# Kernel tuning notes

Measured on AMD Instinct MI355X. Metric: run time of the kernel, lower is better.

The kernel has to match this reference:

```python
import jax, jax.numpy as jnp
import numpy as np
import math

B, S, DIM = 2, 2048, 2048
H, KV, HD = 16, 1, 128  # query heads, kv heads, head dim


def setup_inputs() -> dict:
    key = jax.random.key(0)
    ks = jax.random.split(key, 6)
    std = 0.02
    return {
        "hidden_states": jax.random.normal(ks[0], (B, S, DIM), jnp.float32),
        "attention_mask": jnp.zeros((B, 1, S, S), jnp.float32),
        "wq": jax.random.normal(ks[1], (DIM, H * HD), jnp.float32) * std,
        "bq": jnp.zeros((H * HD,), jnp.float32),
        "wk": jax.random.normal(ks[2], (DIM, KV * HD), jnp.float32) * std,
        "bk": jnp.zeros((KV * HD,), jnp.float32),
        "wv": jax.random.normal(ks[3], (DIM, KV * HD), jnp.float32) * std,
        "bv": jnp.zeros((KV * HD,), jnp.float32),
        "wo": jax.random.normal(ks[4], (H * HD, DIM), jnp.float32) * std,
        "bo": jnp.zeros((DIM,), jnp.float32),
    }


def reference(hidden_states, attention_mask, wq, bq, wk, bk, wv, bv, wo, bo):
    b, s, _ = hidden_states.shape
    q = (hidden_states @ wq + bq).reshape(b, s, H, HD)
    k = (hidden_states @ wk + bk).reshape(b, s, KV, HD)
    v = (hidden_states @ wv + bv).reshape(b, s, KV, HD)
    # [b, h, s, d]
    q = jnp.transpose(q, (0, 2, 1, 3))
    k = jnp.transpose(k, (0, 2, 1, 3))
    v = jnp.transpose(v, (0, 2, 1, 3))
    # broadcast shared KV heads to all query heads (num_kv_heads < num_query_heads)
    repeats = H // KV
    k = jnp.repeat(k, repeats, axis=1)
    v = jnp.repeat(v, repeats, axis=1)
    scores = jnp.einsum('bhqd,bhkd->bhqk', q, k) / math.sqrt(HD)
    scores = scores + attention_mask
    weights = jax.nn.softmax(scores, axis=-1)
    attn = jnp.einsum('bhqk,bhkd->bhqd', weights, v)
    attn = jnp.transpose(attn, (0, 2, 1, 3)).reshape(b, s, H * HD)
    return attn @ wo + bo
```

## Files before the change

### kernel.cpp

```cpp
#include <hip/hip_runtime.h>
#include <hip/hip_bf16.h>
#include <stdint.h>

#define S_LEN 2048
#define DIMSZ 2048
#define NH    16
#define HD    128
#define NQK   2176
#define NQKV  2304
#define NT2   (S_LEN / 128)

typedef short  bf16x8  __attribute__((ext_vector_type(8)));
typedef float  floatx4 __attribute__((ext_vector_type(4)));
typedef float  floatx16 __attribute__((ext_vector_type(16)));
typedef int    intx4   __attribute__((ext_vector_type(4)));
typedef unsigned short u16;

#define mfma32 __builtin_amdgcn_mfma_f32_32x32x16_bf16
#define LOG2E 1.4426950408889634f
#define C_SL2 (0.08838834764831845f * LOG2E)

__device__ __forceinline__ u16 f2bf(float x) {
  unsigned int u = __builtin_bit_cast(unsigned int, x);
  u = (u + 0x7FFFu + ((u >> 16) & 1u)) >> 16;
  return (u16)u;
}
__device__ __forceinline__ float bf2f(unsigned int bits) {
  return __builtin_bit_cast(float, bits << 16);
}

__device__ __forceinline__ int cvtpk(float lo, float hi) {
  int r;
  asm("v_cvt_pk_bf16_f32 %0, %1, %2" : "=v"(r) : "v"(lo), "v"(hi));
  return r;
}

#if __has_builtin(__builtin_amdgcn_exp2f)
__device__ __forceinline__ float fexp2(float x) { return __builtin_amdgcn_exp2f(x); }
#else
__device__ __forceinline__ float fexp2(float x) { return exp2f(x); }
#endif

#if __has_builtin(__builtin_amdgcn_permlane32_swap)
__device__ __forceinline__ void half_swap(int& a, int& b) {
  auto r = __builtin_amdgcn_permlane32_swap(a, b, false, false);
  a = (int)r[0]; b = (int)r[1];
}
__device__ __forceinline__ float red_max32(float x) {
  int xi = __builtin_bit_cast(int, x);
  auto r = __builtin_amdgcn_permlane32_swap(xi, xi, false, false);
  return fmaxf(__builtin_bit_cast(float, (int)r[0]), __builtin_bit_cast(float, (int)r[1]));
}
__device__ __forceinline__ float red_add32(float x) {
  int xi = __builtin_bit_cast(int, x);
  auto r = __builtin_amdgcn_permlane32_swap(xi, xi, false, false);
  return __builtin_bit_cast(float, (int)r[0]) + __builtin_bit_cast(float, (int)r[1]);
}
#else
__device__ __forceinline__ void half_swap(int& a, int& b) {
  int as = __shfl_xor(a, 32);
  int bs = __shfl_xor(b, 32);
  int lane = threadIdx.x & 63;
  int na = (lane < 32) ? a : bs;
  int nb = (lane < 32) ? as : b;
  a = na; b = nb;
}
__device__ __forceinline__ float red_max32(float x) { return fmaxf(x, __shfl_xor(x, 32)); }
__device__ __forceinline__ float red_add32(float x) { return x + __shfl_xor(x, 32); }
#endif

__device__ __forceinline__ void gload16(const void* g, void* l) {
  __builtin_amdgcn_global_load_lds(
      reinterpret_cast<const __attribute__((address_space(1))) void*>(reinterpret_cast<uintptr_t>(g)),
      reinterpret_cast<__attribute__((address_space(3))) void*>(reinterpret_cast<uintptr_t>(l)),
      16, 0, 0);
}

__global__ void k_cvt_bf16(const float* __restrict__ in, u16* __restrict__ out, int n4) {
  int i = blockIdx.x * blockDim.x + threadIdx.x;
  if (i < n4) {
    float4 v = ((const float4*)in)[i];
    ushort4 o;
    o.x = f2bf(v.x); o.y = f2bf(v.y); o.z = f2bf(v.z); o.w = f2bf(v.w);
    ((ushort4*)out)[i] = o;
  }
}

__global__ void k_transpose_qkv(const float* __restrict__ wq, const float* __restrict__ wk,
                                const float* __restrict__ wv, u16* __restrict__ out, int K) {
  __shared__ float t[64][65];
  int orow0 = blockIdx.x * 64;
  int r0 = blockIdx.y * 64;
  const float* src;
  int N, scol0;
  if (orow0 < 2048)      { src = wq; N = 2048; scol0 = orow0; }
  else if (orow0 < NQK)  { src = wk; N = 128;  scol0 = orow0 - 2048; }
  else                   { src = wv; N = 128;  scol0 = orow0 - NQK; }
  int tid = threadIdx.x;
  int lr = tid >> 6;
  int lc = tid & 63;
#pragma unroll
  for (int i = 0; i < 16; ++i) {
    int r = lr + i * 4;
    t[r][lc] = src[(size_t)(r0 + r) * N + scol0 + lc];
  }
  __syncthreads();
#pragma unroll
  for (int i = 0; i < 16; ++i) {
    int r = lr + i * 4;
    out[(size_t)(orow0 + r) * K + r0 + lc] = f2bf(t[lc][r]);
  }
}

__global__ void k_transpose_bf16(const float* __restrict__ in, u16* __restrict__ out,
                                 int K, int N) {
  __shared__ float t[64][65];
  int c0 = blockIdx.x * 64;
  int r0 = blockIdx.y * 64;
  int tid = threadIdx.x;
  int lr = tid >> 6;
  int lc = tid & 63;
#pragma unroll
  for (int i = 0; i < 16; ++i) {
    int r = lr + i * 4;
    t[r][lc] = in[(size_t)(r0 + r) * N + c0 + lc];
  }
  __syncthreads();
#pragma unroll
  for (int i = 0; i < 16; ++i) {
    int r = lr + i * 4;
    out[(size_t)(c0 + r) * K + r0 + lc] = f2bf(t[lc][r]);
  }
}

__global__ void k_bias_concat(const float* __restrict__ bq, const float* __restrict__ bk,
                              const float* __restrict__ bv, float* __restrict__ out) {
  int i = blockIdx.x * 256 + threadIdx.x;
  if (i < NQKV) out[i] = (i < 2048) ? bq[i] : (i < NQK ? bk[i - 2048] : bv[i - NQK]);
}

__device__ __forceinline__ void stage_tile(const u16* __restrict__ G, int ldg, int row0, int kt,
                                           u16* lbase, int wid, int lane) {
#pragma unroll
  for (int i = 0; i < 4; ++i) {
    int c   = (wid * 4 + i) * 64 + lane;
    int row = c >> 3, cin = c & 7;
    int cs  = cin ^ (row & 7);
    const u16* g = G + (size_t)(row0 + row) * ldg + kt * 64 + cs * 8;
    gload16(g, (char*)lbase + (wid * 4 + i) * 1024);
  }
}

template <int OMODE>
__global__ __launch_bounds__(256)
void k_gemm(const u16* __restrict__ A, const u16* __restrict__ Bt,
            const float* __restrict__ bias, void* __restrict__ Cout,
            u16* __restrict__ vt, int M, int N, int K) {
  __shared__ u16 lA[2][128 * 64];
  __shared__ u16 lB[2][128 * 64];
  const int tid = threadIdx.x, lane = tid & 63, wid = tid >> 6;
  const int wm = wid >> 1, wn = wid & 1;
  const int tm = blockIdx.x, tn = blockIdx.y;
  const int nk = K >> 6;

  stage_tile(A, K, tm * 128, 0, lA[0], wid, lane);
  stage_tile(Bt, K, tn * 128, 0, lB[0], wid, lane);
  __syncthreads();

  floatx4 acc[4][4] = {};
  int buf = 0;
  for (int kt = 0; kt < nk; ++kt) {
    if (kt + 1 < nk) {
      stage_tile(A, K, tm * 128, kt + 1, lA[buf ^ 1], wid, lane);
      stage_tile(Bt, K, tn * 128, kt + 1, lB[buf ^ 1], wid, lane);
    }
    const char* pa = (const char*)&lA[buf][0];
    const char* pb = (const char*)&lB[buf][0];
#pragma unroll
    for (int kk = 0; kk < 2; ++kk) {
      bf16x8 af[4], bfr[4];
      int gch = kk * 4 + (lane >> 4);
#pragma unroll
      for (int f = 0; f < 4; ++f) {
        int ra = wm * 64 + f * 16 + (lane & 15);
        af[f]  = *(const bf16x8*)(pa + ra * 128 + ((gch ^ (ra & 7)) << 4));
        int rb = wn * 64 + f * 16 + (lane & 15);
        bfr[f] = *(const bf16x8*)(pb + rb * 128 + ((gch ^ (rb & 7)) << 4));
      }
      __builtin_amdgcn_s_setprio(1);
#pragma unroll
      for (int fm = 0; fm < 4; ++fm)
#pragma unroll
        for (int fn = 0; fn < 4; ++fn)
          acc[fm][fn] = __builtin_amdgcn_mfma_f32_16x16x32_bf16(af[fm], bfr[fn], acc[fm][fn], 0, 0, 0);
      __builtin_amdgcn_s_setprio(0);
    }
    __syncthreads();
    buf ^= 1;
  }

#pragma unroll
  for (int fm = 0; fm < 4; ++fm)
#pragma unroll
    for (int fn = 0; fn < 4; ++fn)
#pragma unroll
      for (int r = 0; r < 4; ++r) {
        int rowg = tm * 128 + wm * 64 + fm * 16 + (lane >> 4) * 4 + r;
        int colg = tn * 128 + wn * 64 + fn * 16 + (lane & 15);
        float v = acc[fm][fn][r] + bias[colg];
        if constexpr (OMODE == 1) {
          ((float*)Cout)[(size_t)rowg * N + colg] = v;
        } else {
          if (colg < 2048) {
            ((u16*)Cout)[(size_t)rowg * N + colg] = f2bf(v * C_SL2);
          } else if (colg < NQK) {
            ((u16*)Cout)[(size_t)rowg * N + colg] = f2bf(v);
          } else {
            int d = colg - NQK;
            int bg = rowg >> 11, s = rowg & 2047;
            vt[((size_t)bg * HD + d) * S_LEN + s] = f2bf(v);
          }
        }
      }
}

__device__ __forceinline__ void stage_kv128(const u16* __restrict__ qkv, const u16* __restrict__ vt,
                                            int b, int kt, u16* lK, u16* lV, int wid, int lane) {
#pragma unroll
  for (int i = 0; i < 4; ++i) {
    int seg = wid * 4 + i;
    int r = seg * 4 + (lane >> 4);
    int cin = lane & 15;
    int cs = cin ^ (r & 15);
    const u16* gk = qkv + (size_t)(b * S_LEN + kt * 128 + r) * NQKV + 2048 + cs * 8;
    gload16(gk, (char*)lK + seg * 1024);
    const u16* gv = vt + ((size_t)b * HD + r) * S_LEN + kt * 128 + cs * 8;
    gload16(gv, (char*)lV + seg * 1024);
  }
}

__device__ __forceinline__ void mask_write128(u16* lMb, int mq, int mc, floatx4 m0, floatx4 m1) {
  intx4 w;
  w[0] = cvtpk(m0[0] * LOG2E, m0[1] * LOG2E);
  w[1] = cvtpk(m0[2] * LOG2E, m0[3] * LOG2E);
  w[2] = cvtpk(m1[0] * LOG2E, m1[1] * LOG2E);
  w[3] = cvtpk(m1[2] * LOG2E, m1[3] * LOG2E);
  *(intx4*)((char*)lMb + mq * 256 + ((mc ^ (mq & 15)) << 4)) = w;
}

__global__ __launch_bounds__(512)
void k_attn(const u16* __restrict__ qkv, const u16* __restrict__ vt,
            const float* __restrict__ mask, u16* __restrict__ attn) {
  __shared__ __align__(16) u16 lK[2][128 * 128];
  __shared__ __align__(16) u16 lV[2][128 * 128];
  __shared__ __align__(16) u16 lMb[2][32 * 128];
  const int tid = threadIdx.x, lane = tid & 63, wid = tid >> 6;
  const int qt = blockIdx.x, hg = blockIdx.y, b = blockIdx.z;
  const int h = hg * 8 + wid;
  const int q = lane & 31, h5 = lane >> 5;

  bf16x8 qf[8];
  const size_t qrow = (size_t)(b * S_LEN + qt * 32 + q);
#pragma unroll
  for (int cs = 0; cs < 8; ++cs)
    qf[cs] = *(const bf16x8*)(qkv + qrow * NQKV + h * HD + cs * 16 + h5 * 8);

  const int qb = q * 256;
  int offK[8], offVc[8], offM[16];
#pragma unroll
  for (int cs = 0; cs < 8; ++cs)
    offK[cs] = qb + (((cs * 2 + h5) ^ (q & 15)) << 4);
#pragma unroll
  for (int hf = 0; hf < 2; ++hf)
#pragma unroll
    for (int ks = 0; ks < 4; ++ks)
      offVc[hf * 4 + ks] = (((hf * 8 + ks * 2 + h5) ^ (q & 15)) << 4);
#pragma unroll
  for (int c = 0; c < 16; ++c)
    offM[c] = qb + ((c ^ (q & 15)) << 4) + h5 * 8;

  float m_ = -1e30f, l_ = 0.f;
  floatx16 acco[4] = {};

  const int mq = tid >> 4, mc = tid & 15;
  const float* mrow = mask + (size_t)b * S_LEN * S_LEN + (size_t)(qt * 32 + mq) * S_LEN + mc * 8;

  stage_kv128(qkv, vt, b, 0, lK[0], lV[0], wid, lane);
  {
    floatx4 m0 = *(const floatx4*)(mrow);
    floatx4 m1 = *(const floatx4*)(mrow + 4);
    mask_write128(&lMb[0][0], mq, mc, m0, m1);
  }
  __syncthreads();

  int buf = 0;
  for (int kt = 0; kt < NT2; ++kt) {
    floatx4 mr0, mr1;
    if (kt + 1 < NT2) {
      stage_kv128(qkv, vt, b, kt + 1, lK[buf ^ 1], lV[buf ^ 1], wid, lane);
      mr0 = *(const floatx4*)(mrow + (size_t)(kt + 1) * 128);
      mr1 = *(const floatx4*)(mrow + (size_t)(kt + 1) * 128 + 4);
    }
    const char* pKb = (const char*)&lK[buf][0];
    const char* pVb = (const char*)&lV[buf][0];
    const char* pMb = (const char*)&lMb[buf][0];

#pragma unroll
    for (int hf = 0; hf < 2; ++hf) {
      floatx16 accs0, accs1;
#pragma unroll
      for (int kb = 0; kb < 2; ++kb)
#pragma unroll
        for (int rg = 0; rg < 4; ++rg) {
          ushort4 mu = *(const ushort4*)(pMb + offM[hf * 8 + kb * 4 + rg]);
          if (kb == 0) {
            accs0[rg * 4 + 0] = bf2f(mu.x);
            accs0[rg * 4 + 1] = bf2f(mu.y);
            accs0[rg * 4 + 2] = bf2f(mu.z);
            accs0[rg * 4 + 3] = bf2f(mu.w);
          } else {
            accs1[rg * 4 + 0] = bf2f(mu.x);
            accs1[rg * 4 + 1] = bf2f(mu.y);
            accs1[rg * 4 + 2] = bf2f(mu.z);
            accs1[rg * 4 + 3] = bf2f(mu.w);
          }
        }

      const char* pK = pKb + hf * 16384;
      __builtin_amdgcn_s_setprio(1);
#pragma unroll
      for (int cs = 0; cs < 8; ++cs) {
        bf16x8 kf0 = *(const bf16x8*)(pK + offK[cs]);
        bf16x8 kf1 = *(const bf16x8*)(pK + 8192 + offK[cs]);
        accs0 = mfma32(kf0, qf[cs], accs0, 0, 0, 0);
        accs1 = mfma32(kf1, qf[cs], accs1, 0, 0, 0);
      }
      __builtin_amdgcn_s_setprio(0);

      float pm0 = -1e30f, pm1 = -1e30f, pm2 = -1e30f, pm3 = -1e30f;
#pragma unroll
      for (int r = 0; r < 16; r += 4) {
        pm0 = fmaxf(fmaxf(accs0[r + 0], accs0[r + 1]), pm0);
        pm1 = fmaxf(fmaxf(accs0[r + 2], accs0[r + 3]), pm1);
        pm2 = fmaxf(fmaxf(accs1[r + 0], accs1[r + 1]), pm2);
        pm3 = fmaxf(fmaxf(accs1[r + 2], accs1[r + 3]), pm3);
      }
      float rowm = red_max32(fmaxf(fmaxf(pm0, pm1), fmaxf(pm2, pm3)));

      if (__any(rowm > m_ + 11.5415603f)) {
        float mn = fmaxf(m_, rowm);
        float al = fexp2(m_ - mn);
        m_ = mn;
        l_ *= al;
#pragma unroll
        for (int dt = 0; dt < 4; ++dt) acco[dt] *= al;
      }
      float pr[32];
      float ps0 = 0.f, ps1 = 0.f, ps2 = 0.f, ps3 = 0.f;
#pragma unroll
      for (int i = 0; i < 16; i += 4) {
        float e0 = fexp2(accs0[i + 0] - m_); pr[i + 0] = e0; ps0 += e0;
        float e1 = fexp2(accs0[i + 1] - m_); pr[i + 1] = e1; ps1 += e1;
        float e2 = fexp2(accs0[i + 2] - m_); pr[i + 2] = e2; ps2 += e2;
        float e3 = fexp2(accs0[i + 3] - m_); pr[i + 3] = e3; ps3 += e3;
      }
#pragma unroll
      for (int i = 0; i < 16; i += 4) {
        float e0 = fexp2(accs1[i + 0] - m_); pr[16 + i + 0] = e0; ps0 += e0;
        float e1 = fexp2(accs1[i + 1] - m_); pr[16 + i + 1] = e1; ps1 += e1;
        float e2 = fexp2(accs1[i + 2] - m_); pr[16 + i + 2] = e2; ps2 += e2;
        float e3 = fexp2(accs1[i + 3] - m_); pr[16 + i + 3] = e3; ps3 += e3;
      }
      l_ += red_add32((ps0 + ps1) + (ps2 + ps3));

      bf16x8 pf[4];
#pragma unroll
      for (int kb = 0; kb < 2; ++kb)
#pragma unroll
        for (int s = 0; s < 2; ++s) {
          int base = kb * 16 + s * 8;
          int A0 = cvtpk(pr[base + 0], pr[base + 1]);
          int A1 = cvtpk(pr[base + 2], pr[base + 3]);
          int B0 = cvtpk(pr[base + 4], pr[base + 5]);
          int B1 = cvtpk(pr[base + 6], pr[base + 7]);
          half_swap(A0, B0);
          half_swap(A1, B1);
          intx4 w;
          w[0] = A0; w[1] = A1; w[2] = B0; w[3] = B1;
          pf[kb * 2 + s] = __builtin_bit_cast(bf16x8, w);
        }

      __builtin_amdgcn_s_setprio(1);
#pragma unroll
      for (int dt = 0; dt < 4; ++dt)
#pragma unroll
        for (int ks = 0; ks < 4; ++ks) {
          bf16x8 vf = *(const bf16x8*)(pVb + dt * 8192 + qb + offVc[hf * 4 + ks]);
          acco[dt] = mfma32(vf, pf[ks], acco[dt], 0, 0, 0);
        }
      __builtin_amdgcn_s_setprio(0);
    }

    if (kt + 1 < NT2)
      mask_write128(&lMb[buf ^ 1][0], mq, mc, mr0, mr1);
    __syncthreads();
    buf ^= 1;
  }

  float inv = 1.0f / l_;
  u16* obase = attn + qrow * DIMSZ + h * HD;
#pragma unroll
  for (int dt = 0; dt < 4; ++dt)
#pragma unroll
    for (int rg = 0; rg < 4; ++rg) {
      int d0 = dt * 32 + rg * 8 + h5 * 4;
      ushort4 st;
      st.x = f2bf(acco[dt][rg * 4 + 0] * inv);
      st.y = f2bf(acco[dt][rg * 4 + 1] * inv);
      st.z = f2bf(acco[dt][rg * 4 + 2] * inv);
      st.w = f2bf(acco[dt][rg * 4 + 3] * inv);
      *(ushort4*)(obase + d0) = st;
    }
}

extern "C" void kernel_launch(void* const* d_in, const int* in_sizes, int n_in,
                              void* d_out, int out_size, void* d_ws, size_t ws_size,
                              hipStream_t stream) {
  const float* hidden = (const float*)d_in[0];
  const float* mask   = (const float*)d_in[1];
  const float* wq = (const float*)d_in[2];
  const float* bq = (const float*)d_in[3];
  const float* wk = (const float*)d_in[4];
  const float* bk = (const float*)d_in[5];
  const float* wv = (const float*)d_in[6];
  const float* bv = (const float*)d_in[7];
  const float* wo = (const float*)d_in[8];
  const float* bo = (const float*)d_in[9];
  float* out = (float*)d_out;

  char* ws = (char*)d_ws;
  u16*   hb    = (u16*)(ws);
  u16*   wqkvT = (u16*)(ws + 16777216);
  u16*   woT   = (u16*)(ws + 26214400);
  float* bqkv  = (float*)(ws + 34603008);
  u16*   qkv   = (u16*)(ws + 34612224);
  u16*   vt    = (u16*)(ws + 53486592);
  u16*   attn  = (u16*)(ws + 54535168);

  k_cvt_bf16<<<dim3(8192), dim3(256), 0, stream>>>(hidden, hb, 4096 * 2048 / 4);
  k_transpose_qkv<<<dim3(36, 32), dim3(256), 0, stream>>>(wq, wk, wv, wqkvT, 2048);
  k_transpose_bf16<<<dim3(32, 32), dim3(256), 0, stream>>>(wo, woT, 2048, 2048);
  k_bias_concat<<<dim3(9), dim3(256), 0, stream>>>(bq, bk, bv, bqkv);

  k_gemm<0><<<dim3(32, 18), dim3(256), 0, stream>>>(hb, wqkvT, bqkv, (void*)qkv, vt, 4096, NQKV, 2048);
  k_attn<<<dim3(64, 2, 2), dim3(512), 0, stream>>>(qkv, vt, mask, attn);
  k_gemm<1><<<dim3(32, 16), dim3(256), 0, stream>>>(attn, woT, bo, (void*)out, (u16*)nullptr, 4096, 2048, 2048);
}
```

Baseline: 199.7 us.

## Fuse prep kernels into one launch and issue all QK MFMAs upfront

After: 192.7 us (median of 2 runs). 1.04x faster.

```diff
diff --git a/kernel.cpp b/kernel.cpp
--- a/kernel.cpp
+++ b/kernel.cpp
@@ -76,29 +76,47 @@
       16, 0, 0);
 }
 
-__global__ void k_cvt_bf16(const float* __restrict__ in, u16* __restrict__ out, int n4) {
-  int i = blockIdx.x * blockDim.x + threadIdx.x;
-  if (i < n4) {
-    float4 v = ((const float4*)in)[i];
+__global__ __launch_bounds__(256)
+void k_prep(const float* __restrict__ hidden, u16* __restrict__ hb,
+            const float* __restrict__ wq, const float* __restrict__ wk,
+            const float* __restrict__ wv, u16* __restrict__ wqkvT,
+            const float* __restrict__ wo, u16* __restrict__ woT,
+            const float* __restrict__ bq, const float* __restrict__ bk,
+            const float* __restrict__ bv, float* __restrict__ bqkv) {
+  __shared__ float t[64][65];
+  int bid = blockIdx.x;
+  int tid = threadIdx.x;
+  if (bid < 8192) {
+    int i = bid * 256 + tid;
+    float4 v = ((const float4*)hidden)[i];
     ushort4 o;
     o.x = f2bf(v.x); o.y = f2bf(v.y); o.z = f2bf(v.z); o.w = f2bf(v.w);
-    ((ushort4*)out)[i] = o;
-  }
-}
-
-__global__ void k_transpose_qkv(const float* __restrict__ wq, const float* __restrict__ wk,
-                                const float* __restrict__ wv, u16* __restrict__ out, int K) {
-  __shared__ float t[64][65];
-  int orow0 = blockIdx.x * 64;
-  int r0 = blockIdx.y * 64;
+    ((ushort4*)hb)[i] = o;
+    return;
+  }
+  bid -= 8192;
   const float* src;
-  int N, scol0;
-  if (orow0 < 2048)      { src = wq; N = 2048; scol0 = orow0; }
-  else if (orow0 < NQK)  { src = wk; N = 128;  scol0 = orow0 - 2048; }
-  else                   { src = wv; N = 128;  scol0 = orow0 - NQK; }
-  int tid = threadIdx.x;
-  int lr = tid >> 6;
-  int lc = tid & 63;
+  u16* dst;
+  int N, scol0, orow0, r0;
+  if (bid < 1152) {
+    orow0 = (bid % 36) * 64;
+    r0 = (bid / 36) * 64;
+    if (orow0 < 2048)      { src = wq; N = 2048; scol0 = orow0; }
+    else if (orow0 < NQK)  { src = wk; N = 128;  scol0 = orow0 - 2048; }
+    else                   { src = wv; N = 128;  scol0 = orow0 - NQK; }
+    dst = wqkvT;
+  } else if (bid < 1152 + 1024) {
+    int b2 = bid - 1152;
+    orow0 = (b2 % 32) * 64;
+    r0 = (b2 / 32) * 64;
+    src = wo; N = 2048; scol0 = orow0;
+    dst = woT;
+  } else {
+    int i = (bid - 1152 - 1024) * 256 + tid;
+    if (i < NQKV) bqkv[i] = (i < 2048) ? bq[i] : (i < NQK ? bk[i - 2048] : bv[i - NQK]);
+    return;
+  }
+  int lr = tid >> 6, lc = tid & 63;
 #pragma unroll
   for (int i = 0; i < 16; ++i) {
     int r = lr + i * 4;
@@ -108,35 +126,8 @@
 #pragma unroll
   for (int i = 0; i < 16; ++i) {
     int r = lr + i * 4;
-    out[(size_t)(orow0 + r) * K + r0 + lc] = f2bf(t[lc][r]);
-  }
-}
-
-__global__ void k_transpose_bf16(const float* __restrict__ in, u16* __restrict__ out,
-                                 int K, int N) {
-  __shared__ float t[64][65];
-  int c0 = blockIdx.x * 64;
-  int r0 = blockIdx.y * 64;
-  int tid = threadIdx.x;
-  int lr = tid >> 6;
-  int lc = tid & 63;
-#pragma unroll
-  for (int i = 0; i < 16; ++i) {
-    int r = lr + i * 4;
-    t[r][lc] = in[(size_t)(r0 + r) * N + c0 + lc];
-  }
-  __syncthreads();
-#pragma unroll
-  for (int i = 0; i < 16; ++i) {
-    int r = lr + i * 4;
-    out[(size_t)(c0 + r) * K + r0 + lc] = f2bf(t[lc][r]);
-  }
-}
-
-__global__ void k_bias_concat(const float* __restrict__ bq, const float* __restrict__ bk,
-                              const float* __restrict__ bv, float* __restrict__ out) {
-  int i = blockIdx.x * 256 + threadIdx.x;
-  if (i < NQKV) out[i] = (i < 2048) ? bq[i] : (i < NQK ? bk[i - 2048] : bv[i - NQK]);
+    dst[(size_t)(orow0 + r) * 2048 + r0 + lc] = f2bf(t[lc][r]);
+  }
 }
 
 __device__ __forceinline__ void stage_tile(const u16* __restrict__ G, int ldg, int row0, int kt,
@@ -305,48 +296,48 @@
     const char* pVb = (const char*)&lV[buf][0];
     const char* pMb = (const char*)&lMb[buf][0];
 
-#pragma unroll
-    for (int hf = 0; hf < 2; ++hf) {
-      floatx16 accs0, accs1;
-#pragma unroll
-      for (int kb = 0; kb < 2; ++kb)
-#pragma unroll
-        for (int rg = 0; rg < 4; ++rg) {
-          ushort4 mu = *(const ushort4*)(pMb + offM[hf * 8 + kb * 4 + rg]);
-          if (kb == 0) {
-            accs0[rg * 4 + 0] = bf2f(mu.x);
-            accs0[rg * 4 + 1] = bf2f(mu.y);
-            accs0[rg * 4 + 2] = bf2f(mu.z);
-            accs0[rg * 4 + 3] = bf2f(mu.w);
-          } else {
-            accs1[rg * 4 + 0] = bf2f(mu.x);
-            accs1[rg * 4 + 1] = bf2f(mu.y);
-            accs1[rg * 4 + 2] = bf2f(mu.z);
-            accs1[rg * 4 + 3] = bf2f(mu.w);
-          }
-        }
-
-      const char* pK = pKb + hf * 16384;
-      __builtin_amdgcn_s_setprio(1);
-#pragma unroll
-      for (int cs = 0; cs < 8; ++cs) {
-        bf16x8 kf0 = *(const bf16x8*)(pK + offK[cs]);
-        bf16x8 kf1 = *(const bf16x8*)(pK + 8192 + offK[cs]);
-        accs0 = mfma32(kf0, qf[cs], accs0, 0, 0, 0);
-        accs1 = mfma32(kf1, qf[cs], accs1, 0, 0, 0);
-      }
-      __builtin_amdgcn_s_setprio(0);
-
+    floatx16 aA0, aA1, aB0, aB1;
+#pragma unroll
+    for (int rg = 0; rg < 4; ++rg) {
+      ushort4 mu;
+      mu = *(const ushort4*)(pMb + offM[0 * 8 + 0 * 4 + rg]);
+      aA0[rg * 4 + 0] = bf2f(mu.x); aA0[rg * 4 + 1] = bf2f(mu.y);
+      aA0[rg * 4 + 2] = bf2f(mu.z); aA0[rg * 4 + 3] = bf2f(mu.w);
+      mu = *(const ushort4*)(pMb + offM[0 * 8 + 1 * 4 + rg]);
+      aA1[rg * 4 + 0] = bf2f(mu.x); aA1[rg * 4 + 1] = bf2f(mu.y);
+      aA1[rg * 4 + 2] = bf2f(mu.z); aA1[rg * 4 + 3] = bf2f(mu.w);
+      mu = *(const ushort4*)(pMb + offM[1 * 8 + 0 * 4 + rg]);
+      aB0[rg * 4 + 0] = bf2f(mu.x); aB0[rg * 4 + 1] = bf2f(mu.y);
+      aB0[rg * 4 + 2] = bf2f(mu.z); aB0[rg * 4 + 3] = bf2f(mu.w);
+      mu = *(const ushort4*)(pMb + offM[1 * 8 + 1 * 4 + rg]);
+      aB1[rg * 4 + 0] = bf2f(mu.x); aB1[rg * 4 + 1] = bf2f(mu.y);
+      aB1[rg * 4 + 2] = bf2f(mu.z); aB1[rg * 4 + 3] = bf2f(mu.w);
+    }
+
+    __builtin_amdgcn_s_setprio(1);
+#pragma unroll
+    for (int cs = 0; cs < 8; ++cs) {
+      bf16x8 k0 = *(const bf16x8*)(pKb + offK[cs]);
+      bf16x8 k1 = *(const bf16x8*)(pKb + 8192 + offK[cs]);
+      bf16x8 k2 = *(const bf16x8*)(pKb + 16384 + offK[cs]);
+      bf16x8 k3 = *(const bf16x8*)(pKb + 24576 + offK[cs]);
+      aA0 = mfma32(k0, qf[cs], aA0, 0, 0, 0);
+      aA1 = mfma32(k1, qf[cs], aA1, 0, 0, 0);
+      aB0 = mfma32(k2, qf[cs], aB0, 0, 0, 0);
+      aB1 = mfma32(k3, qf[cs], aB1, 0, 0, 0);
+    }
+    __builtin_amdgcn_s_setprio(0);
+
+    {
       float pm0 = -1e30f, pm1 = -1e30f, pm2 = -1e30f, pm3 = -1e30f;
 #pragma unroll
       for (int r = 0; r < 16; r += 4) {
-        pm0 = fmaxf(fmaxf(accs0[r + 0], accs0[r + 1]), pm0);
-        pm1 = fmaxf(fmaxf(accs0[r + 2], accs0[r + 3]), pm1);
-        pm2 = fmaxf(fmaxf(accs1[r + 0], accs1[r + 1]), pm2);
-        pm3 = fmaxf(fmaxf(accs1[r + 2], accs1[r + 3]), pm3);
+        pm0 = fmaxf(fmaxf(aA0[r + 0], aA0[r + 1]), pm0);
+        pm1 = fmaxf(fmaxf(aA0[r + 2], aA0[r + 3]), pm1);
+        pm2 = fmaxf(fmaxf(aA1[r + 0], aA1[r + 1]), pm2);
+        pm3 = fmaxf(fmaxf(aA1[r + 2], aA1[r + 3]), pm3);
       }
       float rowm = red_max32(fmaxf(fmaxf(pm0, pm1), fmaxf(pm2, pm3)));
-
       if (__any(rowm > m_ + 11.5415603f)) {
         float mn = fmaxf(m_, rowm);
         float al = fexp2(m_ - mn);
@@ -359,17 +350,17 @@
       float ps0 = 0.f, ps1 = 0.f, ps2 = 0.f, ps3 = 0.f;
 #pragma unroll
       for (int i = 0; i < 16; i += 4) {
-        float e0 = fexp2(accs0[i + 0] - m_); pr[i + 0] = e0; ps0 += e0;
-        float e1 = fexp2(accs0[i + 1] - m_); pr[i + 1] = e1; ps1 += e1;
-        float e2 = fexp2(accs0[i + 2] - m_); pr[i + 2] = e2; ps2 += e2;
-        float e3 = fexp2(accs0[i + 3] - m_); pr[i + 3] = e3; ps3 += e3;
+        float e0 = fexp2(aA0[i + 0] - m_); pr[i + 0] = e0; ps0 += e0;
+        float e1 = fexp2(aA0[i + 1] - m_); pr[i + 1] = e1; ps1 += e1;
+        float e2 = fexp2(aA0[i + 2] - m_); pr[i + 2] = e2; ps2 += e2;
+        float e3 = fexp2(aA0[i + 3] - m_); pr[i + 3] = e3; ps3 += e3;
       }
 #pragma unroll
       for (int i = 0; i < 16; i += 4) {
-        float e0 = fexp2(accs1[i + 0] - m_); pr[16 + i + 0] = e0; ps0 += e0;
-        float e1 = fexp2(accs1[i + 1] - m_); pr[16 + i + 1] = e1; ps1 += e1;
-        float e2 = fexp2(accs1[i + 2] - m_); pr[16 + i + 2] = e2; ps2 += e2;
-        float e3 = fexp2(accs1[i + 3] - m_); pr[16 + i + 3] = e3; ps3 += e3;
+        float e0 = fexp2(aA1[i + 0] - m_); pr[16 + i + 0] = e0; ps0 += e0;
+        float e1 = fexp2(aA1[i + 1] - m_); pr[16 + i + 1] = e1; ps1 += e1;
+        float e2 = fexp2(aA1[i + 2] - m_); pr[16 + i + 2] = e2; ps2 += e2;
+        float e3 = fexp2(aA1[i + 3] - m_); pr[16 + i + 3] = e3; ps3 += e3;
       }
       l_ += red_add32((ps0 + ps1) + (ps2 + ps3));
 
@@ -395,7 +386,71 @@
       for (int dt = 0; dt < 4; ++dt)
 #pragma unroll
         for (int ks = 0; ks < 4; ++ks) {
-          bf16x8 vf = *(const bf16x8*)(pVb + dt * 8192 + qb + offVc[hf * 4 + ks]);
+          bf16x8 vf = *(const bf16x8*)(pVb + dt * 8192 + qb + offVc[ks]);
+          acco[dt] = mfma32(vf, pf[ks], acco[dt], 0, 0, 0);
+        }
+      __builtin_amdgcn_s_setprio(0);
+    }
+
+    {
+      float pm0 = -1e30f, pm1 = -1e30f, pm2 = -1e30f, pm3 = -1e30f;
+#pragma unroll
+      for (int r = 0; r < 16; r += 4) {
+        pm0 = fmaxf(fmaxf(aB0[r + 0], aB0[r + 1]), pm0);
+        pm1 = fmaxf(fmaxf(aB0[r + 2], aB0[r + 3]), pm1);
+        pm2 = fmaxf(fmaxf(aB1[r + 0], aB1[r + 1]), pm2);
+        pm3 = fmaxf(fmaxf(aB1[r + 2], aB1[r + 3]), pm3);
+      }
+      float rowm = red_max32(fmaxf(fmaxf(pm0, pm1), fmaxf(pm2, pm3)));
+      if (__any(rowm > m_ + 11.5415603f)) {
+        float mn = fmaxf(m_, rowm);
+        float al = fexp2(m_ - mn);
+        m_ = mn;
+        l_ *= al;
+#pragma unroll
+        for (int dt = 0; dt < 4; ++dt) acco[dt] *= al;
+      }
+      float pr[32];
+      float ps0 = 0.f, ps1 = 0.f, ps2 = 0.f, ps3 = 0.f;
+#pragma unroll
+      for (int i = 0; i < 16; i += 4) {
+        float e0 = fexp2(aB0[i + 0] - m_); pr[i + 0] = e0; ps0 += e0;
+        float e1 = fexp2(aB0[i + 1] - m_); pr[i + 1] = e1; ps1 += e1;
+        float e2 = fexp2(aB0[i + 2] - m_); pr[i + 2] = e2; ps2 += e2;
+        float e3 = fexp2(aB0[i + 3] - m_); pr[i + 3] = e3; ps3 += e3;
+      }
+#pragma unroll
+      for (int i = 0; i < 16; i += 4) {
+        float e0 = fexp2(aB1[i + 0] - m_); pr[16 + i + 0] = e0; ps0 += e0;
+        float e1 = fexp2(aB1[i + 1] - m_); pr[16 + i + 1] = e1; ps1 += e1;
+        float e2 = fexp2(aB1[i + 2] - m_); pr[16 + i + 2] = e2; ps2 += e2;
+        float e3 = fexp2(aB1[i + 3] - m_); pr[16 + i + 3] = e3; ps3 += e3;
+      }
+      l_ += red_add32((ps0 + ps1) + (ps2 + ps3));
+
+      bf16x8 pf[4];
+#pragma unroll
+      for (int kb = 0; kb < 2; ++kb)
+#pragma unroll
+        for (int s = 0; s < 2; ++s) {
+          int base = kb * 16 + s * 8;
+          int A0 = cvtpk(pr[base + 0], pr[base + 1]);
+          int A1 = cvtpk(pr[base + 2], pr[base + 3]);
+          int B0 = cvtpk(pr[base + 4], pr[base + 5]);
+          int B1 = cvtpk(pr[base + 6], pr[base + 7]);
+          half_swap(A0, B0);
+          half_swap(A1, B1);
+          intx4 w;
+          w[0] = A0; w[1] = A1; w[2] = B0; w[3] = B1;
+          pf[kb * 2 + s] = __builtin_bit_cast(bf16x8, w);
+        }
+
+      __builtin_amdgcn_s_setprio(1);
+#pragma unroll
+      for (int dt = 0; dt < 4; ++dt)
+#pragma unroll
+        for (int ks = 0; ks < 4; ++ks) {
+          bf16x8 vf = *(const bf16x8*)(pVb + dt * 8192 + qb + offVc[4 + ks]);
           acco[dt] = mfma32(vf, pf[ks], acco[dt], 0, 0, 0);
         }
       __builtin_amdgcn_s_setprio(0);
@@ -447,11 +502,8 @@
   u16*   vt    = (u16*)(ws + 53486592);
   u16*   attn  = (u16*)(ws + 54535168);
 
-  k_cvt_bf16<<<dim3(8192), dim3(256), 0, stream>>>(hidden, hb, 4096 * 2048 / 4);
-  k_transpose_qkv<<<dim3(36, 32), dim3(256), 0, stream>>>(wq, wk, wv, wqkvT, 2048);
-  k_transpose_bf16<<<dim3(32, 32), dim3(256), 0, stream>>>(wo, woT, 2048, 2048);
-  k_bias_concat<<<dim3(9), dim3(256), 0, stream>>>(bq, bk, bv, bqkv);
-
+  k_prep<<<dim3(10377), dim3(256), 0, stream>>>(hidden, hb, wq, wk, wv, wqkvT,
+                                                wo, woT, bq, bk, bv, bqkv);
   k_gemm<0><<<dim3(32, 18), dim3(256), 0, stream>>>(hb, wqkvT, bqkv, (void*)qkv, vt, 4096, NQKV, 2048);
   k_attn<<<dim3(64, 2, 2), dim3(512), 0, stream>>>(qkv, vt, mask, attn);
   k_gemm<1><<<dim3(32, 16), dim3(256), 0, stream>>>(attn, woT, bo, (void*)out, (u16*)nullptr, 4096, 2048, 2048);
```
